# Optimization experiments

Hardware: AMD Instinct MI355X
Metric: run time of the kernel (lower is better)

Reference implementation:

```python
import jax, jax.numpy as jnp
import numpy as np

N = 8192      # nodes
F = 256       # in_features
H = 64        # hidden_dim
NEG = -9e15   # mask fill value from the torch source
EPS = 1e-5    # LayerNorm eps (torch default)


def setup_inputs() -> dict:
    key = jax.random.key(0)
    ks = jax.random.split(key, 6)
    x = jax.random.normal(ks[0], (N, F), jnp.float32)
    adj = jax.random.randint(ks[1], (N, N), 0, 2, jnp.int32)
    # Linear params (xavier-ish scale, zero bias as in reset_parameters)
    Wt = jax.random.normal(ks[2], (H, F), jnp.float32) * (1.0 / np.sqrt(F))
    bt = jnp.zeros((H,), jnp.float32)
    Wa = jax.random.normal(ks[3], (1, H), jnp.float32) * (1.0 / np.sqrt(H))
    ba = jnp.zeros((1,), jnp.float32)
    Wp = jax.random.normal(ks[4], (F, H), jnp.float32) * (1.0 / np.sqrt(H))
    bp = jnp.zeros((F,), jnp.float32)
    gamma = jnp.ones((F,), jnp.float32)
    beta = jnp.zeros((F,), jnp.float32)
    return dict(x=x, adj=adj, Wt=Wt, bt=bt, Wa=Wa, ba=ba,
                Wp=Wp, bp=bp, gamma=gamma, beta=beta)


def reference(x, adj, Wt, bt, Wa, ba, Wp, bp, gamma, beta):
    # h = feature_transform(x): [N, H]
    h = x @ Wt.T + bt
    # per-source-node scalar score, expanded over all N columns: [N, 1]
    s = jax.nn.leaky_relu(h @ Wa.T + ba, negative_slope=0.2)
    # adjacency-masked softmax over neighbors (dim=1); s broadcasts to [N, N]
    scores = jnp.where(adj > 0, s, jnp.float32(NEG))
    w = jax.nn.softmax(scores, axis=1)            # [N, N]
    # dropout inactive at inference -> identity
    neighbor = w @ h                               # [N, H]
    tf = neighbor @ Wp.T + bp                      # [N, F]
    # residual + LayerNorm
    y = x + tf
    mu = jnp.mean(y, axis=-1, keepdims=True)
    var = jnp.var(y, axis=-1, keepdims=True)
    return gamma * (y - mu) * jax.lax.rsqrt(var + EPS) + beta
```

## Files before the change

kernel.cpp:

```cpp
#include <hip/hip_runtime.h>
#include <stdint.h>

#define NN 8192
#define FF 256
#define HH 64

typedef __attribute__((ext_vector_type(8))) short bf16x8;
typedef __attribute__((ext_vector_type(4))) float f32x4;

__device__ __forceinline__ uint16_t f2bf(float f) {
  union { float f; uint32_t i; } c; c.f = f;
  uint32_t r = c.i + 0x7FFFu + ((c.i >> 16) & 1u);
  return (uint16_t)(r >> 16);
}

__global__ __launch_bounds__(256) void k1_h(
    const float* __restrict__ x, const float* __restrict__ Wt,
    const float* __restrict__ bt, float* __restrict__ h) {
  __shared__ float wtT[256 * 65];
  __shared__ float sbt[64];
  const int t = threadIdx.x;
  const int lane = t & 63;
  const int w = t >> 6;

  for (int i = 0; i < 64; ++i)
    wtT[t * 65 + i] = Wt[(size_t)i * FF + t];
  if (t < 64) sbt[t] = bt[t];
  __syncthreads();

  const int r0 = blockIdx.x * 32 + w * 8;
  const float binit = sbt[lane];
  float acc[8];
#pragma unroll
  for (int r = 0; r < 8; ++r) acc[r] = binit;

  for (int f4 = 0; f4 < FF; f4 += 4) {
    float4 xs[8];
#pragma unroll
    for (int r = 0; r < 8; ++r)
      xs[r] = *(const float4*)(x + (size_t)(r0 + r) * FF + f4);
    const float wt0 = wtT[(f4 + 0) * 65 + lane];
    const float wt1 = wtT[(f4 + 1) * 65 + lane];
    const float wt2 = wtT[(f4 + 2) * 65 + lane];
    const float wt3 = wtT[(f4 + 3) * 65 + lane];
#pragma unroll
    for (int r = 0; r < 8; ++r)
      acc[r] += xs[r].x * wt0 + xs[r].y * wt1 + xs[r].z * wt2 + xs[r].w * wt3;
  }
#pragma unroll
  for (int r = 0; r < 8; ++r)
    h[(size_t)(r0 + r) * HH + lane] = acc[r];
}

__global__ __launch_bounds__(256) void k1b_hT(
    const float* __restrict__ h, uint16_t* __restrict__ hT) {
  __shared__ float s[64][65];
  const int t = threadIdx.x;
  const int n0 = blockIdx.x * 64;
  for (int i = 0; i < 16; ++i) {
    int idx = i * 256 + t;
    int r = idx >> 6, c = idx & 63;
    s[r][c] = h[(size_t)(n0 + r) * HH + c];
  }
  __syncthreads();
  for (int i = 0; i < 16; ++i) {
    int idx = i * 256 + t;
    int c = idx >> 6, n = idx & 63;
    hT[(size_t)c * NN + n0 + n] = f2bf(s[n][c]);
  }
}

__global__ __launch_bounds__(256) void k2_attn(
    const float* __restrict__ x, const int* __restrict__ adj,
    const uint16_t* __restrict__ hT, const float* __restrict__ Wp,
    const float* __restrict__ bp, const float* __restrict__ gamma,
    const float* __restrict__ beta, float* __restrict__ out) {
  __shared__ float s_part[4][16][64];
  __shared__ float s_nb[16][64];
  __shared__ float s_y[16 * 256];
  __shared__ int   s_deg[16];

  const int t    = threadIdx.x;
  const int w    = t >> 6;
  const int lane = t & 63;
  const int m    = lane & 15;
  const int q    = lane >> 4;
  const int row0 = blockIdx.x * 16;

  if (t < 16) s_deg[t] = 0;
  __syncthreads();

  const int kbeg = w * (NN / 4);
  const int kend = kbeg + (NN / 4);

  f32x4 acc0 = 0, acc1 = 0, acc2 = 0, acc3 = 0;
  int degm = 0;
  const int* __restrict__ arow = adj + (size_t)(row0 + m) * NN;
  const uint16_t* __restrict__ hrow = hT + (size_t)m * NN;

  for (int kb = kbeg; kb < kend; kb += 64) {
    const int k0 = kb + q * 8;
    const int k1 = k0 + 32;
    int4 a0 = *(const int4*)(arow + k0);
    int4 a1 = *(const int4*)(arow + k0 + 4);
    int4 a2 = *(const int4*)(arow + k1);
    int4 a3 = *(const int4*)(arow + k1 + 4);
    bf16x8 b0 = *(const bf16x8*)(hrow + k0);
    bf16x8 b1 = *(const bf16x8*)(hrow + 16 * NN + k0);
    bf16x8 b2 = *(const bf16x8*)(hrow + 32 * NN + k0);
    bf16x8 b3 = *(const bf16x8*)(hrow + 48 * NN + k0);
    bf16x8 c0 = *(const bf16x8*)(hrow + k1);
    bf16x8 c1 = *(const bf16x8*)(hrow + 16 * NN + k1);
    bf16x8 c2 = *(const bf16x8*)(hrow + 32 * NN + k1);
    bf16x8 c3 = *(const bf16x8*)(hrow + 48 * NN + k1);
    bf16x8 afA;
    afA[0] = a0.x ? (short)0x3F80 : (short)0;
    afA[1] = a0.y ? (short)0x3F80 : (short)0;
    afA[2] = a0.z ? (short)0x3F80 : (short)0;
    afA[3] = a0.w ? (short)0x3F80 : (short)0;
    afA[4] = a1.x ? (short)0x3F80 : (short)0;
    afA[5] = a1.y ? (short)0x3F80 : (short)0;
    afA[6] = a1.z ? (short)0x3F80 : (short)0;
    afA[7] = a1.w ? (short)0x3F80 : (short)0;
    bf16x8 afB;
    afB[0] = a2.x ? (short)0x3F80 : (short)0;
    afB[1] = a2.y ? (short)0x3F80 : (short)0;
    afB[2] = a2.z ? (short)0x3F80 : (short)0;
    afB[3] = a2.w ? (short)0x3F80 : (short)0;
    afB[4] = a3.x ? (short)0x3F80 : (short)0;
    afB[5] = a3.y ? (short)0x3F80 : (short)0;
    afB[6] = a3.z ? (short)0x3F80 : (short)0;
    afB[7] = a3.w ? (short)0x3F80 : (short)0;
    acc0 = __builtin_amdgcn_mfma_f32_16x16x32_bf16(afA, b0, acc0, 0, 0, 0);
    acc1 = __builtin_amdgcn_mfma_f32_16x16x32_bf16(afA, b1, acc1, 0, 0, 0);
    acc2 = __builtin_amdgcn_mfma_f32_16x16x32_bf16(afA, b2, acc2, 0, 0, 0);
    acc3 = __builtin_amdgcn_mfma_f32_16x16x32_bf16(afA, b3, acc3, 0, 0, 0);
    acc0 = __builtin_amdgcn_mfma_f32_16x16x32_bf16(afB, c0, acc0, 0, 0, 0);
    acc1 = __builtin_amdgcn_mfma_f32_16x16x32_bf16(afB, c1, acc1, 0, 0, 0);
    acc2 = __builtin_amdgcn_mfma_f32_16x16x32_bf16(afB, c2, acc2, 0, 0, 0);
    acc3 = __builtin_amdgcn_mfma_f32_16x16x32_bf16(afB, c3, acc3, 0, 0, 0);
    degm += a0.x + a0.y + a0.z + a0.w + a1.x + a1.y + a1.z + a1.w;
    degm += a2.x + a2.y + a2.z + a2.w + a3.x + a3.y + a3.z + a3.w;
  }

  degm += __shfl_down(degm, 32, 64);
  degm += __shfl_down(degm, 16, 64);
  if (lane < 16) atomicAdd(&s_deg[lane], degm);

#pragma unroll
  for (int rg = 0; rg < 4; ++rg) {
    s_part[w][q * 4 + rg][ 0 + m] = acc0[rg];
    s_part[w][q * 4 + rg][16 + m] = acc1[rg];
    s_part[w][q * 4 + rg][32 + m] = acc2[rg];
    s_part[w][q * 4 + rg][48 + m] = acc3[rg];
  }
  __syncthreads();

  for (int idx = t; idx < 16 * 64; idx += 256) {
    int r = idx >> 6, c = idx & 63;
    float s = s_part[0][r][c] + s_part[1][r][c] +
              s_part[2][r][c] + s_part[3][r][c];
    int d = s_deg[r];
    s_nb[r][c] = (d > 0) ? s / (float)d : 0.f;
  }
  __syncthreads();

  {
    const int f = t;
    float wp[64];
    const float* wrow = Wp + (size_t)f * HH;
#pragma unroll
    for (int j = 0; j < 16; ++j) {
      float4 v = *(const float4*)(wrow + j * 4);
      wp[j * 4 + 0] = v.x; wp[j * 4 + 1] = v.y;
      wp[j * 4 + 2] = v.z; wp[j * 4 + 3] = v.w;
    }
    const float bpf = bp[f];
    for (int r = 0; r < 16; ++r) {
      float a = bpf;
#pragma unroll
      for (int k = 0; k < 64; k += 4) {
        float4 nv = *(const float4*)&s_nb[r][k];
        a += nv.x * wp[k] + nv.y * wp[k + 1] + nv.z * wp[k + 2] + nv.w * wp[k + 3];
      }
      float y = x[(size_t)(row0 + r) * FF + f] + a;
      s_y[r * 256 + f] = y;
    }
  }
  __syncthreads();

  for (int i = 0; i < 4; ++i) {
    const int r = w * 4 + i;
    float4 v = *(const float4*)&s_y[r * 256 + lane * 4];
    float sum = v.x + v.y + v.z + v.w;
    float ss  = v.x * v.x + v.y * v.y + v.z * v.z + v.w * v.w;
#pragma unroll
    for (int o = 32; o >= 1; o >>= 1) {
      sum += __shfl_xor(sum, o, 64);
      ss  += __shfl_xor(ss, o, 64);
    }
    const float mu  = sum * (1.0f / 256.0f);
    const float var = ss * (1.0f / 256.0f) - mu * mu;
    const float rs  = rsqrtf(var + 1e-5f);
    const int f0 = lane * 4;
    float4 g = *(const float4*)(gamma + f0);
    float4 b = *(const float4*)(beta + f0);
    float4 o4;
    o4.x = g.x * (v.x - mu) * rs + b.x;
    o4.y = g.y * (v.y - mu) * rs + b.y;
    o4.z = g.z * (v.z - mu) * rs + b.z;
    o4.w = g.w * (v.w - mu) * rs + b.w;
    *(float4*)(out + (size_t)(row0 + r) * FF + f0) = o4;
  }
}

extern "C" void kernel_launch(void* const* d_in, const int* in_sizes, int n_in,
                              void* d_out, int out_size, void* d_ws, size_t ws_size,
                              hipStream_t stream) {
  const float* x     = (const float*)d_in[0];
  const int*   adj   = (const int*)d_in[1];
  const float* Wt    = (const float*)d_in[2];
  const float* bt    = (const float*)d_in[3];
  const float* Wp    = (const float*)d_in[6];
  const float* bp    = (const float*)d_in[7];
  const float* gamma = (const float*)d_in[8];
  const float* beta  = (const float*)d_in[9];
  float* out = (float*)d_out;
  float*    h  = (float*)d_ws;
  uint16_t* hT = (uint16_t*)((char*)d_ws + (size_t)NN * HH * 4);

  k1_h  <<<256, 256, 0, stream>>>(x, Wt, bt, h);
  k1b_hT<<<128, 256, 0, stream>>>(h, hT);
  k2_attn<<<512, 256, 0, stream>>>(x, adj, hT, Wp, bp, gamma, beta, out);
}
```

Before: 447.0 us.

## Split attention reduction across two blocks per row group with atomic accumulation

The attention kernel now splits the K dimension of each 16-row group across two blocks, doubling the grid to 1024 blocks. Partial neighbor sums and degrees are accumulated into global buffers with atomics, and those buffers are zeroed in the first kernel. The projection, residual and LayerNorm epilogue moves into a separate kernel. The goal is more blocks in flight to saturate bandwidth on the 256 MB adjacency read, at the cost of an extra launch, global atomics and a round trip of partial sums through global memory.

```diff
diff --git a/kernel.cpp b/kernel.cpp
--- a/kernel.cpp
+++ b/kernel.cpp
@@ -16,7 +16,8 @@
 
 __global__ __launch_bounds__(256) void k1_h(
     const float* __restrict__ x, const float* __restrict__ Wt,
-    const float* __restrict__ bt, float* __restrict__ h) {
+    const float* __restrict__ bt, float* __restrict__ h,
+    float* __restrict__ nb_sum, int* __restrict__ deg_g) {
   __shared__ float wtT[256 * 65];
   __shared__ float sbt[64];
   const int t = threadIdx.x;
@@ -50,6 +51,11 @@
 #pragma unroll
   for (int r = 0; r < 8; ++r)
     h[(size_t)(r0 + r) * HH + lane] = acc[r];
+
+  float4 z = {0.f, 0.f, 0.f, 0.f};
+  float4* nbz = (float4*)(nb_sum + (size_t)blockIdx.x * 32 * HH);
+  for (int i = t; i < 512; i += 256) nbz[i] = z;
+  if (t < 32) deg_g[blockIdx.x * 32 + t] = 0;
 }
 
 __global__ __launch_bounds__(256) void k1b_hT(
@@ -71,13 +77,9 @@
 }
 
 __global__ __launch_bounds__(256) void k2_attn(
-    const float* __restrict__ x, const int* __restrict__ adj,
-    const uint16_t* __restrict__ hT, const float* __restrict__ Wp,
-    const float* __restrict__ bp, const float* __restrict__ gamma,
-    const float* __restrict__ beta, float* __restrict__ out) {
+    const int* __restrict__ adj, const uint16_t* __restrict__ hT,
+    float* __restrict__ nb_sum, int* __restrict__ deg_g) {
   __shared__ float s_part[4][16][64];
-  __shared__ float s_nb[16][64];
-  __shared__ float s_y[16 * 256];
   __shared__ int   s_deg[16];
 
   const int t    = threadIdx.x;
@@ -85,13 +87,15 @@
   const int lane = t & 63;
   const int m    = lane & 15;
   const int q    = lane >> 4;
-  const int row0 = blockIdx.x * 16;
+  const int g    = blockIdx.x >> 1;
+  const int half = blockIdx.x & 1;
+  const int row0 = g * 16;
 
   if (t < 16) s_deg[t] = 0;
   __syncthreads();
 
-  const int kbeg = w * (NN / 4);
-  const int kend = kbeg + (NN / 4);
+  const int kbeg = half * (NN / 2) + w * (NN / 8);
+  const int kend = kbeg + (NN / 8);
 
   f32x4 acc0 = 0, acc1 = 0, acc2 = 0, acc3 = 0;
   int degm = 0;
@@ -160,7 +164,28 @@
     int r = idx >> 6, c = idx & 63;
     float s = s_part[0][r][c] + s_part[1][r][c] +
               s_part[2][r][c] + s_part[3][r][c];
-    int d = s_deg[r];
+    atomicAdd(&nb_sum[(size_t)(row0 + r) * HH + c], s);
+  }
+  if (t < 16) atomicAdd(&deg_g[row0 + t], s_deg[t]);
+}
+
+__global__ __launch_bounds__(256) void k3_epi(
+    const float* __restrict__ x, const float* __restrict__ nb_sum,
+    const int* __restrict__ deg_g, const float* __restrict__ Wp,
+    const float* __restrict__ bp, const float* __restrict__ gamma,
+    const float* __restrict__ beta, float* __restrict__ out) {
+  __shared__ float s_nb[16][64];
+  __shared__ float s_y[16 * 256];
+
+  const int t    = threadIdx.x;
+  const int w    = t >> 6;
+  const int lane = t & 63;
+  const int row0 = blockIdx.x * 16;
+
+  for (int idx = t; idx < 16 * 64; idx += 256) {
+    int r = idx >> 6, c = idx & 63;
+    int d = deg_g[row0 + r];
+    float s = nb_sum[(size_t)(row0 + r) * HH + c];
     s_nb[r][c] = (d > 0) ? s / (float)d : 0.f;
   }
   __syncthreads();
@@ -226,10 +251,14 @@
   const float* gamma = (const float*)d_in[8];
   const float* beta  = (const float*)d_in[9];
   float* out = (float*)d_out;
-  float*    h  = (float*)d_ws;
-  uint16_t* hT = (uint16_t*)((char*)d_ws + (size_t)NN * HH * 4);
-
-  k1_h  <<<256, 256, 0, stream>>>(x, Wt, bt, h);
+
+  uint16_t* hT     = (uint16_t*)d_ws;
+  float*    nb_sum = (float*)((char*)d_ws + (1u << 20));
+  int*      deg_g  = (int*)((char*)d_ws + (3u << 20));
+  float*    h      = (float*)((char*)d_ws + (3u << 20) + (1u << 18));
+
+  k1_h  <<<256, 256, 0, stream>>>(x, Wt, bt, h, nb_sum, deg_g);
   k1b_hT<<<128, 256, 0, stream>>>(h, hT);
-  k2_attn<<<512, 256, 0, stream>>>(x, adj, hT, Wp, bp, gamma, beta, out);
-}
+  k2_attn<<<1024, 256, 0, stream>>>(adj, hT, nb_sum, deg_g);
+  k3_epi<<<512, 256, 0, stream>>>(x, nb_sum, deg_g, Wp, bp, gamma, beta, out);
+}
```

Result: no change. 440.7 us (-1.4%).
